# Kernel tuning notes

Hardware: AMD Instinct MI355X
Metric: run time of the kernel (lower is better)

Reference implementation:

```python
import jax, jax.numpy as jnp
import numpy as np

N = 131072      # nodes
E = 524288      # edges (avg degree 4)
F_IN = 16       # node features (QM9-like)
DIM = 64        # GRU hidden / lin0 out
DNN = 16        # NNConv channels
BK = 4          # bond kinds (edge_attr dim)
NG = 8192       # graphs in batch
NL1 = 4         # number of GRUs
NL2 = 2         # inner repeats per GRU


def setup_inputs() -> dict:
    key = jax.random.key(0)
    ks = jax.random.split(key, 16)
    s = 0.1
    inp = {}
    inp["x"] = jax.random.normal(ks[0], (N, F_IN), jnp.float32)
    inp["edge_attr"] = jax.random.uniform(ks[1], (E, BK), dtype=jnp.float32)
    # lin0: F_IN -> DIM
    inp["lin0_w"] = jax.random.normal(ks[2], (F_IN, DIM), jnp.float32) * s
    inp["lin0_b"] = jnp.zeros((DIM,), jnp.float32)
    # nn1: BK -> DNN*DNN (per-edge weight generator)
    inp["nn1_w"] = jax.random.normal(ks[3], (BK, DNN * DNN), jnp.float32) * s
    inp["nn1_b"] = jax.random.normal(ks[4], (DNN * DNN,), jnp.float32) * s
    # NNConv root weight + bias
    inp["root_w"] = jax.random.normal(ks[5], (DNN, DNN), jnp.float32) * s
    inp["conv_b"] = jnp.zeros((DNN,), jnp.float32)
    # 4 GRUs, each input=DNN, hidden=DIM (torch layout: [3*DIM, in])
    inp["gru_w_ih"] = jax.random.normal(ks[6], (NL1, 3 * DIM, DNN), jnp.float32) * s
    inp["gru_w_hh"] = jax.random.normal(ks[7], (NL1, 3 * DIM, DIM), jnp.float32) * s
    inp["gru_b_ih"] = jax.random.normal(ks[8], (NL1, 3 * DIM), jnp.float32) * s
    inp["gru_b_hh"] = jax.random.normal(ks[9], (NL1, 3 * DIM), jnp.float32) * s
    # lin1_64_16 and lin_64_1 (no bias)
    inp["lin1_w"] = jax.random.normal(ks[10], (DIM, DNN), jnp.float32) * s
    inp["lin1_b"] = jnp.zeros((DNN,), jnp.float32)
    inp["lin2_w"] = jax.random.normal(ks[11], (DIM, 1), jnp.float32) * s
    inp["edge_index"] = jax.random.randint(ks[12], (2, E), 0, N, jnp.int32)
    inp["batch"] = jnp.sort(jax.random.randint(ks[13], (N,), 0, NG, jnp.int32))
    return inp


def reference(x, edge_attr, lin0_w, lin0_b, nn1_w, nn1_b, root_w, conv_b,
              gru_w_ih, gru_w_hh, gru_b_ih, gru_b_hh, lin1_w, lin1_b, lin2_w,
              edge_index, batch):
    n = x.shape[0]
    src, dst = edge_index[0], edge_index[1]
    # precompute mean-aggregation denominators (in-degree, clamped at 1)
    cnt = jax.ops.segment_sum(jnp.ones((edge_index.shape[1],), x.dtype), dst,
                              num_segments=n)
    inv_cnt = (1.0 / jnp.maximum(cnt, 1.0))[:, None]          # [N,1]
    # per-edge 16x16 weights from edge features (shared across all iterations)
    W_e = (edge_attr @ nn1_w + nn1_b).reshape(-1, DNN, DNN)   # [E,16,16]

    def nnconv(xi):  # xi: [N,16]
        msg = jnp.einsum('ei,eio->eo', xi[src], W_e)          # gather + per-edge matmul
        aggr = jax.ops.segment_sum(msg, dst, num_segments=n) * inv_cnt  # scatter-mean
        return xi @ root_w + aggr + conv_b

    def gru_step(j, xin, h):  # xin: [N,16], h: [N,64]
        gi = xin @ gru_w_ih[j].T + gru_b_ih[j]                # [N,192]
        gh = h @ gru_w_hh[j].T + gru_b_hh[j]                  # [N,192]
        i_r, i_z, i_n = jnp.split(gi, 3, axis=-1)
        h_r, h_z, h_n = jnp.split(gh, 3, axis=-1)
        r = jax.nn.sigmoid(i_r + h_r)
        z = jax.nn.sigmoid(i_z + h_z)
        ncand = jnp.tanh(i_n + r * h_n)
        return (1.0 - z) * ncand + z * h

    out = jax.nn.relu(x @ lin0_w + lin0_b)                    # [N,64]
    h = out
    for j in range(NL1):
        for _ in range(NL2):
            out1 = out @ lin1_w + lin1_b                      # [N,16]
            out2 = nnconv(out1)                               # [N,16]
            h = gru_step(j, out2, h)
            out = h
    y = out @ lin2_w                                          # [N,1]
    pooled = jax.ops.segment_sum(y, batch, num_segments=NG)   # global_add_pool
    return pooled.reshape(-1)
```

## Files before the change

### kernel.cpp

```cpp
#include <hip/hip_runtime.h>
#include <hip/hip_bf16.h>

#define N_NODES 131072
#define N_EDGES 524288
#define F_IN 16
#define DIM 64
#define DNN 16
#define BK 4
#define NG 8192
#define N_ITERS 8

typedef __bf16 bf16x8 __attribute__((ext_vector_type(8)));
typedef __bf16 bf16x4 __attribute__((ext_vector_type(4)));
typedef float f32x4 __attribute__((ext_vector_type(4)));

#define FMA4(A_, S_, W_) { (A_).x = fmaf((S_), (W_).x, (A_).x); (A_).y = fmaf((S_), (W_).y, (A_).y); \
                           (A_).z = fmaf((S_), (W_).z, (A_).z); (A_).w = fmaf((S_), (W_).w, (A_).w); }

__device__ __forceinline__ unsigned bf16_rne(float f) {
    unsigned u = __float_as_uint(f);
    return (u + 0x7fffu + ((u >> 16) & 1u)) >> 16;
}

__global__ __launch_bounds__(256) void k_degree(const int* __restrict__ ei, int* __restrict__ cnt) {
    int e = blockIdx.x * 256 + threadIdx.x;
    atomicAdd(&cnt[ei[N_EDGES + e]], 1);
}

__global__ __launch_bounds__(256) void k_hist(const int* __restrict__ cnt, int* __restrict__ hist) {
    __shared__ int lh[32];
    int tid = threadIdx.x;
    if (tid < 32) lh[tid] = 0;
    __syncthreads();
    int n = blockIdx.x * 256 + tid;
    int key = 31 - min(cnt[n], 31);
    atomicAdd(&lh[key], 1);
    __syncthreads();
    if (tid < 32 && lh[tid]) atomicAdd(&hist[tid], lh[tid]);
}

__global__ __launch_bounds__(64) void k_binoff(const int* __restrict__ hist, int* __restrict__ binoff) {
    if (threadIdx.x == 0) {
        int acc = 0;
#pragma unroll
        for (int i = 0; i < 32; ++i) { binoff[i] = acc; acc += hist[i]; }
    }
}

__global__ __launch_bounds__(256) void k_permute(const int* __restrict__ cnt, const int* __restrict__ binoff,
                                                 int* __restrict__ bincur, const int* __restrict__ batch,
                                                 int* __restrict__ slot_of, int* __restrict__ cnts,
                                                 float* __restrict__ invs, int* __restrict__ batchs) {
    __shared__ int lh[32], lbase[32];
    int tid = threadIdx.x;
    if (tid < 32) lh[tid] = 0;
    __syncthreads();
    int n = blockIdx.x * 256 + tid;
    int deg = cnt[n];
    int key = 31 - min(deg, 31);
    int myrank = atomicAdd(&lh[key], 1);
    __syncthreads();
    if (tid < 32) lbase[tid] = lh[tid] ? atomicAdd(&bincur[tid], lh[tid]) : 0;
    __syncthreads();
    int slot = binoff[key] + lbase[key] + myrank;
    slot_of[n] = slot;
    cnts[slot] = deg;
    invs[slot] = 1.0f / (float)max(deg, 1);
    batchs[slot] = batch[n];
}

__global__ __launch_bounds__(256) void k_scanA(const int* __restrict__ cnt, int* __restrict__ excl,
                                               int* __restrict__ bsum) {
    __shared__ int a[256], b[256];
    int t = threadIdx.x, gid = blockIdx.x * 256 + t;
    int c = cnt[gid];
    a[t] = c; __syncthreads();
    int *s = a, *d = b;
#pragma unroll
    for (int off = 1; off < 256; off <<= 1) {
        d[t] = s[t] + (t >= off ? s[t - off] : 0);
        __syncthreads();
        int* tmp = s; s = d; d = tmp;
    }
    excl[gid] = s[t] - c;
    if (t == 255) bsum[blockIdx.x] = s[255];
}

__global__ __launch_bounds__(256) void k_scanB(const int* __restrict__ bsum, int* __restrict__ boff) {
    __shared__ int a[512], b[512];
    int t = threadIdx.x;
    a[t] = bsum[t]; a[t + 256] = bsum[t + 256];
    __syncthreads();
    int *s = a, *d = b;
#pragma unroll
    for (int off = 1; off < 512; off <<= 1) {
        d[t] = s[t] + (t >= off ? s[t - off] : 0);
        int i2 = t + 256;
        d[i2] = s[i2] + (i2 >= off ? s[i2 - off] : 0);
        __syncthreads();
        int* tmp = s; s = d; d = tmp;
    }
    boff[t] = t ? s[t - 1] : 0;
    boff[t + 256] = s[t + 255];
}

__global__ __launch_bounds__(256) void k_scanC(const int* __restrict__ excl, const int* __restrict__ boff,
                                               int* __restrict__ row_ptr, int* __restrict__ cursor) {
    int gid = blockIdx.x * 256 + threadIdx.x;
    int v = excl[gid] + boff[gid >> 8];
    row_ptr[gid] = v;
    cursor[gid] = v;
    if (gid == 0) row_ptr[N_NODES] = N_EDGES;
}

__global__ __launch_bounds__(256) void k_scatter(const int* __restrict__ ei, const float* __restrict__ ea,
                                                 const int* __restrict__ slot_of,
                                                 int* __restrict__ cursor, int4* __restrict__ csr_pk) {
    int e = blockIdx.x * 256 + threadIdx.x;
    int ds = slot_of[ei[N_EDGES + e]];
    int pos = atomicAdd(&cursor[ds], 1);
    float4 a = ((const float4*)ea)[e];
    unsigned a01 = bf16_rne(a.x) | (bf16_rne(a.y) << 16);
    unsigned a23 = bf16_rne(a.z) | (bf16_rne(a.w) << 16);
    csr_pk[pos] = make_int4(slot_of[ei[e]], (int)a01, (int)a23, 0);
}

#define WB_SZ (4 * 40 * 512)
__global__ __launch_bounds__(256) void k_prep(const float* __restrict__ wih, const float* __restrict__ whh,
                                              const float* __restrict__ rw, const float* __restrict__ w1,
                                              const float* __restrict__ bih, const float* __restrict__ bhh,
                                              const float* __restrict__ nn1w, const float* __restrict__ nn1b,
                                              __bf16* __restrict__ Wb, __bf16* __restrict__ B2b,
                                              __bf16* __restrict__ w1b) {
    int idx = blockIdx.x * 256 + threadIdx.x;
    if (idx < WB_SZ) {
        int j = idx / 20480, r = idx % 20480;
        int t = r >> 9, e = r & 511;
        int jj = e & 7, c16 = (e >> 3) & 15, kq = e >> 7;
        int ct, kk; bool nih = false;
        if (t < 36) { ct = t / 3; kk = t % 3; } else { ct = 8 + (t - 36); kk = 0; nih = true; }
        int k = kk * 32 + kq * 8 + jj;
        int c = ct * 16 + c16;
        bool ngate = ct >= 8;
        float v = 0.f;
        if (nih) {
            if (k < 16) v = wih[((size_t)j * 192 + c) * 16 + k];
        } else {
            if (k < 16) v = ngate ? 0.f : wih[((size_t)j * 192 + c) * 16 + k];
            else if (k < 80) v = whh[((size_t)j * 192 + c) * 64 + (k - 16)];
            else if (k == 80) v = ngate ? bhh[j * 192 + c] : (bih[j * 192 + c] + bhh[j * 192 + c]);
        }
        Wb[idx] = (__bf16)v;
    } else if (idx < WB_SZ + 1536) {
        int e = idx - WB_SZ;
        int t = e >> 9, ee = e & 511;
        int jj = ee & 7, c16 = (ee >> 3) & 15, kq = ee >> 7;
        int krow = t * 32 + kq * 8 + jj;
        float v;
        if (krow < 16) v = rw[krow * 16 + c16];
        else {
            int i = (krow - 16) >> 4, kk = (krow - 16) & 15;
            v = (i == 0) ? nn1b[kk * 16 + c16] : nn1w[(i - 1) * 256 + kk * 16 + c16];
        }
        B2b[e] = (__bf16)v;
    } else if (idx < WB_SZ + 1536 + 1024) {
        int e = idx - (WB_SZ + 1536);
        int t2 = e >> 9, ee = e & 511;
        int jj = ee & 7, c16 = (ee >> 3) & 15, kq = ee >> 7;
        int k = t2 * 32 + kq * 8 + jj;
        w1b[e] = (__bf16)w1[k * 16 + c16];
    }
}

__global__ __launch_bounds__(256) void k_init(const float* __restrict__ x, const float* __restrict__ w,
                                              const float* __restrict__ b, const int* __restrict__ slot_of,
                                              __bf16* __restrict__ h) {
    __shared__ float s_w[F_IN * DIM];
    int tid = threadIdx.x;
    for (int i = tid; i < F_IN * DIM; i += 256) s_w[i] = w[i];
    int node = blockIdx.x * 16 + (tid >> 4);
    int c4 = tid & 15;
    const float4* xp = (const float4*)(x + (size_t)node * F_IN);
    float4 x0 = xp[0], x1 = xp[1], x2 = xp[2], x3 = xp[3];
    float xa[16] = {x0.x, x0.y, x0.z, x0.w, x1.x, x1.y, x1.z, x1.w,
                    x2.x, x2.y, x2.z, x2.w, x3.x, x3.y, x3.z, x3.w};
    __syncthreads();
    float4 acc = ((const float4*)b)[c4];
    const float4* w4 = (const float4*)s_w;
#pragma unroll
    for (int k = 0; k < 16; ++k) {
        float4 wv = w4[k * 16 + c4];
        FMA4(acc, xa[k], wv);
    }
    bf16x4 hv;
    hv[0] = (__bf16)fmaxf(acc.x, 0.f); hv[1] = (__bf16)fmaxf(acc.y, 0.f);
    hv[2] = (__bf16)fmaxf(acc.z, 0.f); hv[3] = (__bf16)fmaxf(acc.w, 0.f);
    int s = slot_of[node];
    *(bf16x4*)&h[(size_t)s * DIM + c4 * 4] = hv;
}

__global__ __launch_bounds__(256) void k_lin1(const __bf16* __restrict__ h, const float* __restrict__ w,
                                              const float* __restrict__ b, __bf16* __restrict__ out1) {
    __shared__ float s_h[64 * 68];
    int tid = threadIdx.x;
    int nb = blockIdx.x * 64;
    for (int i = tid; i < 64 * 16; i += 256) {
        int n = i >> 4, q4 = i & 15;
        bf16x4 v = *(const bf16x4*)&h[(size_t)(nb + n) * 64 + q4 * 4];
        float* d = &s_h[n * 68 + q4 * 4];
        d[0] = (float)v[0]; d[1] = (float)v[1]; d[2] = (float)v[2]; d[3] = (float)v[3];
    }
    int ct = tid & 15;
    float wcol[64];
#pragma unroll
    for (int q = 0; q < 64; ++q) wcol[q] = w[q * 16 + ct];
    float bias = b[ct];
    __syncthreads();
    int ng = tid >> 4;
#pragma unroll
    for (int rep = 0; rep < 4; ++rep) {
        int nl = ng + 16 * rep;
        float acc = bias;
#pragma unroll
        for (int q4 = 0; q4 < 16; ++q4) {
            float4 hv = *(const float4*)&s_h[nl * 68 + q4 * 4];
            acc = fmaf(hv.x, wcol[4 * q4 + 0], acc);
            acc = fmaf(hv.y, wcol[4 * q4 + 1], acc);
            acc = fmaf(hv.z, wcol[4 * q4 + 2], acc);
            acc = fmaf(hv.w, wcol[4 * q4 + 3], acc);
        }
        out1[(size_t)(nb + nl) * 16 + ct] = (__bf16)acc;
    }
}

__attribute__((amdgpu_waves_per_eu(2, 4)))
__global__ __launch_bounds__(512) void k_node(
    const __bf16* __restrict__ out1_in, __bf16* __restrict__ out1_out,
    const int4* __restrict__ csr_pk,
    const int* __restrict__ row_ptr, const float* __restrict__ invs,
    __bf16* __restrict__ h, const __bf16* __restrict__ Wb, const __bf16* __restrict__ B2b,
    const __bf16* __restrict__ w1b, const float* __restrict__ conv_b,
    const float* __restrict__ bih, const float* __restrict__ lin1_b,
    const int* __restrict__ batchs, const float* __restrict__ lin2_w,
    float* __restrict__ out, int do_final)
{
    __shared__ __align__(16) __bf16 s_X[128 * 104];
    __shared__ __align__(16) __bf16 s_W[40 * 512];
    __shared__ __align__(16) __bf16 s_B2[3 * 512];
    __shared__ __align__(16) __bf16 s_w1[1024];
    int tid = threadIdx.x;
    int nb = blockIdx.x * 128;
    int lane = tid & 63, w = tid >> 6;
    int c16 = lane & 15, lq = lane >> 4;
    int nwb = nb + w * 16;
    int xrow = w * 16;

    {
        const float4* src = (const float4*)Wb;
        float4* dst = (float4*)s_W;
#pragma unroll
        for (int i = 0; i < 5; ++i) dst[tid + 512 * i] = src[tid + 512 * i];
        if (tid < 192) ((float4*)s_B2)[tid] = ((const float4*)B2b)[tid];
        else if (tid < 320) ((float4*)s_w1)[tid - 192] = ((const float4*)w1b)[tid - 192];
    }
    {
        int n = lane >> 2, k4 = lane & 3;
        bf16x4 v = *(const bf16x4*)&out1_in[(size_t)(nwb + n) * 16 + k4 * 4];
        *(bf16x4*)&s_X[(xrow + n) * 104 + k4 * 4] = v;
    }
    __syncthreads();

    {
        int gi = lane >> 4, k = lane & 15;
        int e0[4], dr[4];
        int4 pk[4];
        float S0[4] = {0.f,0.f,0.f,0.f}, S1[4] = {0.f,0.f,0.f,0.f}, S2[4] = {0.f,0.f,0.f,0.f},
              S3[4] = {0.f,0.f,0.f,0.f}, S4[4] = {0.f,0.f,0.f,0.f};
        int rounds = 0;
#pragma unroll
        for (int r = 0; r < 4; ++r) {
            int n = nwb + gi * 4 + r;
            e0[r] = row_ptr[n];
            dr[r] = row_ptr[n + 1] - e0[r];
            rounds = max(rounds, dr[r]);
            pk[r] = csr_pk[min(e0[r], N_EDGES - 1)];
        }
        for (int t = 0; t < rounds; ++t) {
            int4 pkn[4]; float xv[4];
#pragma unroll
            for (int r = 0; r < 4; ++r)
                pkn[r] = csr_pk[min(e0[r] + t + 1, N_EDGES - 1)];
#pragma unroll
            for (int r = 0; r < 4; ++r)
                xv[r] = (float)out1_in[(size_t)(pk[r].x & 0xFFFFF) * 16 + k];
#pragma unroll
            for (int r = 0; r < 4; ++r) {
                float xm = (t < dr[r]) ? xv[r] : 0.0f;
                float a0 = __uint_as_float(((unsigned)pk[r].y) << 16);
                float a1 = __uint_as_float(((unsigned)pk[r].y) & 0xffff0000u);
                float a2 = __uint_as_float(((unsigned)pk[r].z) << 16);
                float a3 = __uint_as_float(((unsigned)pk[r].z) & 0xffff0000u);
                S0[r] += xm;
                S1[r] = fmaf(a0, xm, S1[r]);
                S2[r] = fmaf(a1, xm, S2[r]);
                S3[r] = fmaf(a2, xm, S3[r]);
                S4[r] = fmaf(a3, xm, S4[r]);
                pk[r] = pkn[r];
            }
        }
#pragma unroll
        for (int r = 0; r < 4; ++r) {
            int nl = xrow + gi * 4 + r;
            float inv = invs[nwb + gi * 4 + r];
            __bf16* p = &s_X[nl * 104];
            p[16 + k] = (__bf16)(S0[r] * inv);
            p[32 + k] = (__bf16)(S1[r] * inv);
            p[48 + k] = (__bf16)(S2[r] * inv);
            p[64 + k] = (__bf16)(S3[r] * inv);
            p[80 + k] = (__bf16)(S4[r] * inv);
        }
    }

    float cb = conv_b[c16];
    f32x4 co2 = (f32x4){cb, cb, cb, cb};
#pragma unroll
    for (int kk = 0; kk < 3; ++kk) {
        bf16x8 a = *(const bf16x8*)&s_X[(xrow + c16) * 104 + kk * 32 + lq * 8];
        bf16x8 b = *(const bf16x8*)&s_B2[kk * 512 + lane * 8];
        co2 = __builtin_amdgcn_mfma_f32_16x16x32_bf16(a, b, co2, 0, 0, 0);
    }

#pragma unroll
    for (int jr = 0; jr < 4; ++jr)
        s_X[(xrow + 4 * lq + jr) * 104 + c16] = (__bf16)co2[jr];
    {
        const bf16x8* hsrc = (const bf16x8*)(h + (size_t)nwb * 64);
#pragma unroll
        for (int ii = 0; ii < 2; ++ii) {
            int idx = lane + 64 * ii;
            int n = idx >> 3, d8 = idx & 7;
            bf16x8 v = hsrc[idx];
            *(bf16x8*)&s_X[(xrow + n) * 104 + 16 + d8 * 8] = v;
        }
    }
    {
        int n = lane >> 2, c0 = 80 + (lane & 3) * 4;
#pragma unroll
        for (int q = 0; q < 4; ++q)
            s_X[(xrow + n) * 104 + c0 + q] = (c0 + q == 80) ? (__bf16)1.0f : (__bf16)0.0f;
    }

    f32x4 acc[12], ani4[4];
#pragma unroll
    for (int i = 0; i < 12; ++i) acc[i] = (f32x4){0.f, 0.f, 0.f, 0.f};
#pragma unroll
    for (int i = 0; i < 4; ++i) ani4[i] = (f32x4){0.f, 0.f, 0.f, 0.f};
    bf16x8 af[3];
#pragma unroll
    for (int kk = 0; kk < 3; ++kk)
        af[kk] = *(const bf16x8*)&s_X[(xrow + c16) * 104 + kk * 32 + lq * 8];
#pragma unroll
    for (int ct = 0; ct < 12; ++ct) {
#pragma unroll
        for (int kk = 0; kk < 3; ++kk) {
            bf16x8 bf = *(const bf16x8*)&s_W[(ct * 3 + kk) * 512 + lane * 8];
            acc[ct] = __builtin_amdgcn_mfma_f32_16x16x32_bf16(af[kk], bf, acc[ct], 0, 0, 0);
        }
    }
#pragma unroll
    for (int ct8 = 0; ct8 < 4; ++ct8) {
        bf16x8 bf = *(const bf16x8*)&s_W[(36 + ct8) * 512 + lane * 8];
        ani4[ct8] = __builtin_amdgcn_mfma_f32_16x16x32_bf16(af[0], bf, ani4[ct8], 0, 0, 0);
    }

    float hn[4][4];
#pragma unroll
    for (int ct = 0; ct < 4; ++ct) {
        float bni = bih[128 + ct * 16 + c16];
#pragma unroll
        for (int jr = 0; jr < 4; ++jr) {
            float hold = (float)s_X[(xrow + 4 * lq + jr) * 104 + 16 + ct * 16 + c16];
            float rr = 1.f / (1.f + __expf(-acc[ct][jr]));
            float zz = 1.f / (1.f + __expf(-acc[4 + ct][jr]));
            float xx = fmaf(rr, acc[8 + ct][jr], ani4[ct][jr] + bni);
            float ax = fabsf(xx);
            float ee = __expf(-2.f * ax);
            float ncv = __builtin_copysignf((1.f - ee) / (1.f + ee), xx);
            hn[ct][jr] = fmaf(zz, hold - ncv, ncv);
        }
    }
#pragma unroll
    for (int ct = 0; ct < 4; ++ct)
#pragma unroll
        for (int jr = 0; jr < 4; ++jr)
            s_X[(xrow + 4 * lq + jr) * 104 + 16 + ct * 16 + c16] = (__bf16)hn[ct][jr];
    {
        bf16x8* hdst = (bf16x8*)(h + (size_t)nwb * 64);
#pragma unroll
        for (int ii = 0; ii < 2; ++ii) {
            int idx = lane + 64 * ii;
            int n = idx >> 3, d8 = idx & 7;
            bf16x8 v = *(const bf16x8*)&s_X[(xrow + n) * 104 + 16 + d8 * 8];
            hdst[idx] = v;
        }
    }

    if (!do_final) {
        f32x4 o1acc = (f32x4){0.f, 0.f, 0.f, 0.f};
#pragma unroll
        for (int kk = 0; kk < 2; ++kk) {
            bf16x8 a = *(const bf16x8*)&s_X[(xrow + c16) * 104 + 16 + kk * 32 + lq * 8];
            bf16x8 b = *(const bf16x8*)&s_w1[kk * 512 + lane * 8];
            o1acc = __builtin_amdgcn_mfma_f32_16x16x32_bf16(a, b, o1acc, 0, 0, 0);
        }
        float lb = lin1_b[c16];
#pragma unroll
        for (int jr = 0; jr < 4; ++jr) {
            int node = nwb + 4 * lq + jr;
            out1_out[(size_t)node * 16 + c16] = (__bf16)(o1acc[jr] + lb);
        }
    } else {
        float w2v[4];
#pragma unroll
        for (int ct = 0; ct < 4; ++ct) w2v[ct] = lin2_w[ct * 16 + c16];
#pragma unroll
        for (int jr = 0; jr < 4; ++jr) {
            float part = hn[0][jr] * w2v[0];
            part = fmaf(hn[1][jr], w2v[1], part);
            part = fmaf(hn[2][jr], w2v[2], part);
            part = fmaf(hn[3][jr], w2v[3], part);
#pragma unroll
            for (int off = 8; off > 0; off >>= 1) part += __shfl_xor(part, off, 64);
            if (c16 == 0) {
                int node = nwb + 4 * lq + jr;
                atomicAdd(&out[batchs[node]], part);
            }
        }
    }
}

extern "C" void kernel_launch(void* const* d_in, const int* in_sizes, int n_in,
                              void* d_out, int out_size, void* d_ws, size_t ws_size,
                              hipStream_t stream) {
    const float* x        = (const float*)d_in[0];
    const float* edge_attr= (const float*)d_in[1];
    const float* lin0_w   = (const float*)d_in[2];
    const float* lin0_b   = (const float*)d_in[3];
    const float* nn1_w    = (const float*)d_in[4];
    const float* nn1_b    = (const float*)d_in[5];
    const float* root_w   = (const float*)d_in[6];
    const float* conv_b   = (const float*)d_in[7];
    const float* gru_w_ih = (const float*)d_in[8];
    const float* gru_w_hh = (const float*)d_in[9];
    const float* gru_b_ih = (const float*)d_in[10];
    const float* gru_b_hh = (const float*)d_in[11];
    const float* lin1_w   = (const float*)d_in[12];
    const float* lin1_b   = (const float*)d_in[13];
    const float* lin2_w   = (const float*)d_in[14];
    const int*   ei       = (const int*)d_in[15];
    const int*   batch    = (const int*)d_in[16];
    float* out = (float*)d_out;

    char* p = (char*)d_ws;
    __bf16* h       = (__bf16*)p;           p += (size_t)N_NODES * DIM * 2;
    __bf16* out1A   = (__bf16*)p;           p += (size_t)N_NODES * DNN * 2;
    __bf16* out1B   = (__bf16*)p;           p += (size_t)N_NODES * DNN * 2;
    int4*   csr_pk  = (int4*)p;             p += (size_t)N_EDGES * 16;
    __bf16* Wb      = (__bf16*)p;           p += (size_t)WB_SZ * 2;
    __bf16* B2b     = (__bf16*)p;           p += 1536 * 2;
    __bf16* w1b     = (__bf16*)p;           p += 1024 * 2;
    int*    cnt     = (int*)p;              p += (size_t)N_NODES * 4;
    float*  invs    = (float*)p;            p += (size_t)N_NODES * 4;
    int*    row_ptr = (int*)p;              p += (size_t)(N_NODES + 16) * 4;
    int*    cursor  = (int*)p;              p += (size_t)N_NODES * 4;
    int*    excl    = (int*)p;              p += (size_t)N_NODES * 4;
    int*    bsum    = (int*)p;              p += 512 * 4;
    int*    boff    = (int*)p;              p += 512 * 4;
    int*    slot_of = (int*)p;              p += (size_t)N_NODES * 4;
    int*    cnts    = (int*)p;              p += (size_t)N_NODES * 4;
    int*    batchs  = (int*)p;              p += (size_t)N_NODES * 4;
    int*    hist    = (int*)p;              p += 32 * 4;
    int*    binoff  = (int*)p;              p += 32 * 4;
    int*    bincur  = (int*)p;              p += 32 * 4;

    hipMemsetAsync(d_out, 0, (size_t)NG * 4, stream);
    hipMemsetAsync(cnt, 0, (size_t)N_NODES * 4, stream);
    hipMemsetAsync(hist, 0, 32 * 4, stream);
    hipMemsetAsync(bincur, 0, 32 * 4, stream);
    k_prep<<<330, 256, 0, stream>>>(gru_w_ih, gru_w_hh, root_w, lin1_w, gru_b_ih, gru_b_hh,
                                    nn1_w, nn1_b, Wb, B2b, w1b);
    k_degree<<<N_EDGES / 256, 256, 0, stream>>>(ei, cnt);
    k_hist<<<N_NODES / 256, 256, 0, stream>>>(cnt, hist);
    k_binoff<<<1, 64, 0, stream>>>(hist, binoff);
    k_permute<<<N_NODES / 256, 256, 0, stream>>>(cnt, binoff, bincur, batch,
                                                 slot_of, cnts, invs, batchs);
    k_scanA<<<N_NODES / 256, 256, 0, stream>>>(cnts, excl, bsum);
    k_scanB<<<1, 256, 0, stream>>>(bsum, boff);
    k_scanC<<<N_NODES / 256, 256, 0, stream>>>(excl, boff, row_ptr, cursor);
    k_scatter<<<N_EDGES / 256, 256, 0, stream>>>(ei, edge_attr, slot_of, cursor, csr_pk);
    k_init<<<N_NODES / 16, 256, 0, stream>>>(x, lin0_w, lin0_b, slot_of, h);
    k_lin1<<<N_NODES / 64, 256, 0, stream>>>(h, lin1_w, lin1_b, out1A);

    for (int it = 0; it < N_ITERS; ++it) {
        int j = it >> 1;
        const __bf16* o_in = (it & 1) ? out1B : out1A;
        __bf16*       o_out= (it & 1) ? out1A : out1B;
        k_node<<<N_NODES / 128, 512, 0, stream>>>(o_in, o_out, csr_pk, row_ptr, invs,
                                                  h, Wb + (size_t)j * 40 * 512, B2b, w1b,
                                                  conv_b, gru_b_ih + (size_t)j * 192, lin1_b,
                                                  batchs, lin2_w, out, it == N_ITERS - 1 ? 1 : 0);
    }
}
```

Baseline: 367.6 us.

## Deepen gather prefetch, fold memsets into prep kernel, use fast reciprocals

The edge-aggregation loop in k_node now prefetches the packed CSR entries two steps ahead and the gathered neighbor feature one step ahead, to hide gather latency. Three memsets are folded into k_prep, which now launches 512 blocks so it covers N_NODES, removing separate launches. Divisions in the GRU sigmoid and tanh are replaced with hardware approximate reciprocals. In exchange, the deeper prefetch uses more registers, and the approximate reciprocals slightly reduce precision.

Result: faster. 329.9 us (-10.3%).

```diff
diff --git a/kernel.cpp b/kernel.cpp
--- a/kernel.cpp
+++ b/kernel.cpp
@@ -131,8 +131,11 @@
                                               const float* __restrict__ bih, const float* __restrict__ bhh,
                                               const float* __restrict__ nn1w, const float* __restrict__ nn1b,
                                               __bf16* __restrict__ Wb, __bf16* __restrict__ B2b,
-                                              __bf16* __restrict__ w1b) {
+                                              __bf16* __restrict__ w1b, int* __restrict__ cnt,
+                                              int* __restrict__ hist, int* __restrict__ bincur) {
     int idx = blockIdx.x * 256 + threadIdx.x;
+    if (idx < N_NODES) cnt[idx] = 0;
+    if (idx < 32) { hist[idx] = 0; bincur[idx] = 0; }
     if (idx < WB_SZ) {
         int j = idx / 20480, r = idx % 20480;
         int t = r >> 9, e = r & 511;
@@ -273,7 +276,8 @@
     {
         int gi = lane >> 4, k = lane & 15;
         int e0[4], dr[4];
-        int4 pk[4];
+        int4 pk0[4], pk1[4];
+        float xv0[4];
         float S0[4] = {0.f,0.f,0.f,0.f}, S1[4] = {0.f,0.f,0.f,0.f}, S2[4] = {0.f,0.f,0.f,0.f},
               S3[4] = {0.f,0.f,0.f,0.f}, S4[4] = {0.f,0.f,0.f,0.f};
         int rounds = 0;
@@ -283,29 +287,33 @@
             e0[r] = row_ptr[n];
             dr[r] = row_ptr[n + 1] - e0[r];
             rounds = max(rounds, dr[r]);
-            pk[r] = csr_pk[min(e0[r], N_EDGES - 1)];
-        }
+            pk0[r] = csr_pk[min(e0[r], N_EDGES - 1)];
+        }
+#pragma unroll
+        for (int r = 0; r < 4; ++r) pk1[r] = csr_pk[min(e0[r] + 1, N_EDGES - 1)];
+#pragma unroll
+        for (int r = 0; r < 4; ++r) xv0[r] = (float)out1_in[(size_t)(pk0[r].x & 0xFFFFF) * 16 + k];
         for (int t = 0; t < rounds; ++t) {
-            int4 pkn[4]; float xv[4];
+            int4 pk2[4]; float xv1[4];
 #pragma unroll
             for (int r = 0; r < 4; ++r)
-                pkn[r] = csr_pk[min(e0[r] + t + 1, N_EDGES - 1)];
+                pk2[r] = csr_pk[min(e0[r] + t + 2, N_EDGES - 1)];
 #pragma unroll
             for (int r = 0; r < 4; ++r)
-                xv[r] = (float)out1_in[(size_t)(pk[r].x & 0xFFFFF) * 16 + k];
+                xv1[r] = (float)out1_in[(size_t)(pk1[r].x & 0xFFFFF) * 16 + k];
 #pragma unroll
             for (int r = 0; r < 4; ++r) {
-                float xm = (t < dr[r]) ? xv[r] : 0.0f;
-                float a0 = __uint_as_float(((unsigned)pk[r].y) << 16);
-                float a1 = __uint_as_float(((unsigned)pk[r].y) & 0xffff0000u);
-                float a2 = __uint_as_float(((unsigned)pk[r].z) << 16);
-                float a3 = __uint_as_float(((unsigned)pk[r].z) & 0xffff0000u);
+                float xm = (t < dr[r]) ? xv0[r] : 0.0f;
+                float a0 = __uint_as_float(((unsigned)pk0[r].y) << 16);
+                float a1 = __uint_as_float(((unsigned)pk0[r].y) & 0xffff0000u);
+                float a2 = __uint_as_float(((unsigned)pk0[r].z) << 16);
+                float a3 = __uint_as_float(((unsigned)pk0[r].z) & 0xffff0000u);
                 S0[r] += xm;
                 S1[r] = fmaf(a0, xm, S1[r]);
                 S2[r] = fmaf(a1, xm, S2[r]);
                 S3[r] = fmaf(a2, xm, S3[r]);
                 S4[r] = fmaf(a3, xm, S4[r]);
-                pk[r] = pkn[r];
+                pk0[r] = pk1[r]; pk1[r] = pk2[r]; xv0[r] = xv1[r];
             }
         }
 #pragma unroll
@@ -380,12 +388,12 @@
 #pragma unroll
         for (int jr = 0; jr < 4; ++jr) {
             float hold = (float)s_X[(xrow + 4 * lq + jr) * 104 + 16 + ct * 16 + c16];
-            float rr = 1.f / (1.f + __expf(-acc[ct][jr]));
-            float zz = 1.f / (1.f + __expf(-acc[4 + ct][jr]));
+            float rr = __builtin_amdgcn_rcpf(1.f + __expf(-acc[ct][jr]));
+            float zz = __builtin_amdgcn_rcpf(1.f + __expf(-acc[4 + ct][jr]));
             float xx = fmaf(rr, acc[8 + ct][jr], ani4[ct][jr] + bni);
             float ax = fabsf(xx);
             float ee = __expf(-2.f * ax);
-            float ncv = __builtin_copysignf((1.f - ee) / (1.f + ee), xx);
+            float ncv = __builtin_copysignf((1.f - ee) * __builtin_amdgcn_rcpf(1.f + ee), xx);
             hn[ct][jr] = fmaf(zz, hold - ncv, ncv);
         }
     }
@@ -484,11 +492,8 @@
     int*    bincur  = (int*)p;              p += 32 * 4;
 
     hipMemsetAsync(d_out, 0, (size_t)NG * 4, stream);
-    hipMemsetAsync(cnt, 0, (size_t)N_NODES * 4, stream);
-    hipMemsetAsync(hist, 0, 32 * 4, stream);
-    hipMemsetAsync(bincur, 0, 32 * 4, stream);
-    k_prep<<<330, 256, 0, stream>>>(gru_w_ih, gru_w_hh, root_w, lin1_w, gru_b_ih, gru_b_hh,
-                                    nn1_w, nn1_b, Wb, B2b, w1b);
+    k_prep<<<512, 256, 0, stream>>>(gru_w_ih, gru_w_hh, root_w, lin1_w, gru_b_ih, gru_b_hh,
+                                    nn1_w, nn1_b, Wb, B2b, w1b, cnt, hist, bincur);
     k_degree<<<N_EDGES / 256, 256, 0, stream>>>(ei, cnt);
     k_hist<<<N_NODES / 256, 256, 0, stream>>>(cnt, hist);
     k_binoff<<<1, 64, 0, stream>>>(hist, binoff);
```
